# Optimization experiments

Measured on AMD Instinct MI355X. Metric: run time of the kernel, lower is better.

## Reference

```python
import jax, jax.numpy as jnp
import numpy as np

E = 1024
H = 16
DFF = 4 * E
EPS = 1e-5


def layer_norm(x, scale, bias):
    mu = jnp.mean(x, axis=-1, keepdims=True)
    var = jnp.var(x, axis=-1, keepdims=True)
    return (x - mu) * jax.lax.rsqrt(var + EPS) * scale + bias


def setup_inputs() -> dict:
    key = jax.random.key(0)
    ks = jax.random.split(key, 12)
    N, L = 2, 2048
    x = jax.random.normal(ks[0], (N, L, E), dtype=jnp.float32)
    attn_mask = jax.random.randint(ks[1], (N, H, L, L), 0, 2) == 1
    s = 0.02
    return {
        "x": x,
        "attn_mask": attn_mask,
        "ln1_s": jnp.ones((E,), jnp.float32),
        "ln1_b": jnp.zeros((E,), jnp.float32),
        "Wqkv": jax.random.normal(ks[2], (E, 3 * E), jnp.float32) * s,
        "bqkv": jnp.zeros((3 * E,), jnp.float32),
        "Wo": jax.random.normal(ks[3], (E, E), jnp.float32) * s,
        "bo": jnp.zeros((E,), jnp.float32),
        "ln2_s": jnp.ones((E,), jnp.float32),
        "ln2_b": jnp.zeros((E,), jnp.float32),
        "lnf_s": jnp.ones((E,), jnp.float32),
        "lnf_b": jnp.zeros((E,), jnp.float32),
        "W1": jax.random.normal(ks[4], (E, DFF), jnp.float32) * s,
        "b1": jnp.zeros((DFF,), jnp.float32),
        "W2": jax.random.normal(ks[5], (DFF, E), jnp.float32) * s,
        "b2": jnp.zeros((E,), jnp.float32),
    }


def reference(x, attn_mask, ln1_s, ln1_b, Wqkv, bqkv, Wo, bo,
              ln2_s, ln2_b, lnf_s, lnf_b, W1, b1, W2, b2):
    N, L, _ = x.shape
    D = E // H
    # --- self attention (pre-norm) ---
    h = layer_norm(x, ln1_s, ln1_b)
    qkv = h @ Wqkv + bqkv                      # [N,L,3E]
    q, k, v = jnp.split(qkv, 3, axis=-1)
    q = q.reshape(N, L, H, D)
    k = k.reshape(N, L, H, D)
    v = v.reshape(N, L, H, D)
    a = jnp.einsum('nqhd,nkhd->nhqk', q, k) * (D ** -0.5)  # [N,H,L,L]
    a = jnp.where(attn_mask, -jnp.inf, a)
    a = jax.nn.softmax(a, axis=-1)
    o = jnp.einsum('nhqk,nkhd->nqhd', a, v).reshape(N, L, E)
    o = o @ Wo + bo
    x = x + o
    # --- feedforward (norm_2 then FF's internal LN) ---
    h = layer_norm(x, ln2_s, ln2_b)
    h = layer_norm(h, lnf_s, lnf_b)
    h = jax.nn.gelu(h @ W1 + b1, approximate=False) @ W2 + b2
    return x + h
```

## Files before the change

### kernel.cpp

```cpp
#include <hip/hip_runtime.h>
#include <math.h>

#define E_DIM 1024
#define H_HEADS 16
#define D_HEAD 64
#define DFF_DIM 4096
#define L_SEQ 2048
#define N_BATCH 2
#define T_TOK (N_BATCH * L_SEQ)

typedef __attribute__((ext_vector_type(8))) __bf16 bf16x8;
typedef __attribute__((ext_vector_type(4))) float f32x4;

__device__ __forceinline__ unsigned short f2bf(float f) {
  union { float f; unsigned int u; } v; v.f = f;
  unsigned int r = v.u + 0x7fffu + ((v.u >> 16) & 1u);
  return (unsigned short)(r >> 16);
}

__device__ __forceinline__ void gld16(const void* g, void* l) {
  __builtin_amdgcn_global_load_lds(
      (const __attribute__((address_space(1))) unsigned int*)g,
      (__attribute__((address_space(3))) unsigned int*)l, 16, 0, 0);
}

__global__ __launch_bounds__(256) void convert_transpose(
    const float* __restrict__ in, unsigned short* __restrict__ out, int K, int N) {
  __shared__ float tile[32][33];
  int n0 = blockIdx.x * 32, k0 = blockIdx.y * 32;
  int tx = threadIdx.x & 31, ty = threadIdx.x >> 5;
#pragma unroll
  for (int i = 0; i < 32; i += 8)
    tile[ty + i][tx] = in[(size_t)(k0 + ty + i) * N + n0 + tx];
  __syncthreads();
#pragma unroll
  for (int i = 0; i < 32; i += 8)
    out[(size_t)(n0 + ty + i) * K + k0 + tx] = f2bf(tile[tx][ty + i]);
}

__global__ __launch_bounds__(256) void v_transpose(
    const unsigned short* __restrict__ qkv, unsigned short* __restrict__ vtg) {
  __shared__ unsigned short t[64][72];
  int kb = blockIdx.x * 64;
  int nh = blockIdx.y, n = nh >> 4, h = nh & 15;
  int tid = threadIdx.x;
  int r = tid >> 3, ch = tid & 7;
  const size_t TS = 3 * E_DIM;
  const size_t voff = 2 * E_DIM + h * 64;
#pragma unroll
  for (int it = 0; it < 2; it++) {
    int row = r + it * 32;
    uint4 v = *(const uint4*)(qkv + (size_t)(n * L_SEQ + kb + row) * TS + voff + ch * 8);
    *(uint4*)(&t[row][ch * 8]) = v;
  }
  __syncthreads();
#pragma unroll
  for (int it = 0; it < 2; it++) {
    int d = r + it * 32;
    unsigned short tmp[8];
#pragma unroll
    for (int s = 0; s < 8; s++) tmp[s] = t[ch * 8 + s][d];
    *(uint4*)(vtg + ((size_t)nh * 64 + d) * L_SEQ + kb + ch * 8) = *(uint4*)tmp;
  }
}

__device__ __forceinline__ void block_reduce2(float& a, float& b, float* sm, int tid) {
#pragma unroll
  for (int off = 32; off > 0; off >>= 1) {
    a += __shfl_down(a, off);
    b += __shfl_down(b, off);
  }
  int wid = tid >> 6;
  if ((tid & 63) == 0) { sm[wid * 2] = a; sm[wid * 2 + 1] = b; }
  __syncthreads();
  a = sm[0] + sm[2] + sm[4] + sm[6];
  b = sm[1] + sm[3] + sm[5] + sm[7];
}

__global__ __launch_bounds__(256) void ln_kernel(
    const float* __restrict__ x, const float* __restrict__ s,
    const float* __restrict__ b, unsigned short* __restrict__ out) {
  int row = blockIdx.x, tid = threadIdx.x;
  __shared__ float sm[8];
  float4 v = ((const float4*)(x + (size_t)row * E_DIM))[tid];
  float sum = v.x + v.y + v.z + v.w;
  float sq = v.x * v.x + v.y * v.y + v.z * v.z + v.w * v.w;
  block_reduce2(sum, sq, sm, tid);
  float mu = sum * (1.0f / E_DIM);
  float var = sq * (1.0f / E_DIM) - mu * mu;
  float rs = rsqrtf(var + 1e-5f);
  float4 sv = ((const float4*)s)[tid];
  float4 bv = ((const float4*)b)[tid];
  ushort4 o4;
  o4.x = f2bf((v.x - mu) * rs * sv.x + bv.x);
  o4.y = f2bf((v.y - mu) * rs * sv.y + bv.y);
  o4.z = f2bf((v.z - mu) * rs * sv.z + bv.z);
  o4.w = f2bf((v.w - mu) * rs * sv.w + bv.w);
  ((ushort4*)(out + (size_t)row * E_DIM))[tid] = o4;
}

__global__ __launch_bounds__(256) void ln2_fused_kernel(
    const float* __restrict__ p0, const float* __restrict__ p1,
    const float* __restrict__ x, const float* __restrict__ bo,
    const float* __restrict__ s2, const float* __restrict__ b2,
    const float* __restrict__ sf, const float* __restrict__ bf_,
    float* __restrict__ x2, unsigned short* __restrict__ out) {
  int row = blockIdx.x, tid = threadIdx.x;
  __shared__ float sm[8];
  float4 a0 = ((const float4*)(p0 + (size_t)row * E_DIM))[tid];
  float4 a1 = ((const float4*)(p1 + (size_t)row * E_DIM))[tid];
  float4 xv = ((const float4*)(x + (size_t)row * E_DIM))[tid];
  float4 bov = ((const float4*)bo)[tid];
  float4 v;
  v.x = a0.x + a1.x + xv.x + bov.x;
  v.y = a0.y + a1.y + xv.y + bov.y;
  v.z = a0.z + a1.z + xv.z + bov.z;
  v.w = a0.w + a1.w + xv.w + bov.w;
  ((float4*)(x2 + (size_t)row * E_DIM))[tid] = v;
  float sum = v.x + v.y + v.z + v.w;
  float sq = v.x * v.x + v.y * v.y + v.z * v.z + v.w * v.w;
  block_reduce2(sum, sq, sm, tid);
  float mu = sum * (1.0f / E_DIM);
  float rs = rsqrtf(sq * (1.0f / E_DIM) - mu * mu + 1e-5f);
  float4 s2v = ((const float4*)s2)[tid];
  float4 b2v = ((const float4*)b2)[tid];
  float y0 = (v.x - mu) * rs * s2v.x + b2v.x;
  float y1 = (v.y - mu) * rs * s2v.y + b2v.y;
  float y2 = (v.z - mu) * rs * s2v.z + b2v.z;
  float y3 = (v.w - mu) * rs * s2v.w + b2v.w;
  float sum2 = y0 + y1 + y2 + y3;
  float sq2 = y0 * y0 + y1 * y1 + y2 * y2 + y3 * y3;
  __syncthreads();
  block_reduce2(sum2, sq2, sm, tid);
  float mu2 = sum2 * (1.0f / E_DIM);
  float rs2 = rsqrtf(sq2 * (1.0f / E_DIM) - mu2 * mu2 + 1e-5f);
  float4 sfv = ((const float4*)sf)[tid];
  float4 bfv = ((const float4*)bf_)[tid];
  ushort4 o4;
  o4.x = f2bf((y0 - mu2) * rs2 * sfv.x + bfv.x);
  o4.y = f2bf((y1 - mu2) * rs2 * sfv.y + bfv.y);
  o4.z = f2bf((y2 - mu2) * rs2 * sfv.z + bfv.z);
  o4.w = f2bf((y3 - mu2) * rs2 * sfv.w + bfv.w);
  ((ushort4*)(out + (size_t)row * E_DIM))[tid] = o4;
}

__global__ __launch_bounds__(256) void add4_kernel(
    const float* __restrict__ p0, const float* __restrict__ p1,
    const float* __restrict__ p2, const float* __restrict__ p3,
    const float* __restrict__ resid, const float* __restrict__ bias,
    float* __restrict__ out) {
  int row = blockIdx.x, tid = threadIdx.x;
  size_t base = (size_t)row * E_DIM;
  float4 a0 = ((const float4*)(p0 + base))[tid];
  float4 a1 = ((const float4*)(p1 + base))[tid];
  float4 a2 = ((const float4*)(p2 + base))[tid];
  float4 a3 = ((const float4*)(p3 + base))[tid];
  float4 rv = ((const float4*)(resid + base))[tid];
  float4 bv = ((const float4*)bias)[tid];
  float4 o;
  o.x = a0.x + a1.x + a2.x + a3.x + rv.x + bv.x;
  o.y = a0.y + a1.y + a2.y + a3.y + rv.y + bv.y;
  o.z = a0.z + a1.z + a2.z + a3.z + rv.z + bv.z;
  o.w = a0.w + a1.w + a2.w + a3.w + rv.w + bv.w;
  ((float4*)(out + base))[tid] = o;
}

template <int EPI>
__global__ __launch_bounds__(256) void gemm_bt(
    const unsigned short* __restrict__ A, const unsigned short* __restrict__ Bt,
    const float* __restrict__ bias, void* __restrict__ outp,
    int M, int N, int K, int Ks) {
  __shared__ unsigned short As[128 * 32];
  __shared__ unsigned short Bs[128 * 32];
  int tid = threadIdx.x;
  int lane = tid & 63, wave = tid >> 6;
  int m0 = blockIdx.y * 128, n0 = blockIdx.x * 128;
  int kz = blockIdx.z * Ks;
  int wm = (wave & 1) * 64, wn = (wave >> 1) * 64;
  int lm = lane & 15, lq = lane >> 4;
  int srow = wave * 32 + (lane >> 2);
  int scol = (lane & 3) * 8;
  const unsigned short* Ag = A + (size_t)(m0 + srow) * K + scol;
  const unsigned short* Bg = Bt + (size_t)(n0 + srow) * K + scol;
  unsigned short* AsW = As + wave * 1024;
  unsigned short* BsW = Bs + wave * 1024;
  f32x4 acc[4][4] = {};
  for (int k0 = kz; k0 < kz + Ks; k0 += 32) {
    __syncthreads();
    gld16(Ag + k0, AsW);
    gld16(Ag + (size_t)16 * K + k0, AsW + 512);
    gld16(Bg + k0, BsW);
    gld16(Bg + (size_t)16 * K + k0, BsW + 512);
    __syncthreads();
    bf16x8 a[4], b[4];
#pragma unroll
    for (int i = 0; i < 4; i++)
      a[i] = *(const bf16x8*)(As + (wm + i * 16 + lm) * 32 + lq * 8);
#pragma unroll
    for (int j = 0; j < 4; j++)
      b[j] = *(const bf16x8*)(Bs + (wn + j * 16 + lm) * 32 + lq * 8);
#pragma unroll
    for (int i = 0; i < 4; i++)
#pragma unroll
      for (int j = 0; j < 4; j++)
        acc[i][j] = __builtin_amdgcn_mfma_f32_16x16x32_bf16(a[i], b[j], acc[i][j], 0, 0, 0);
  }
  float* pout = (EPI == 3) ? ((float*)outp + (size_t)blockIdx.z * M * N) : nullptr;
#pragma unroll
  for (int i = 0; i < 4; i++)
#pragma unroll
    for (int j = 0; j < 4; j++) {
      int row = m0 + wm + i * 16 + lq * 4;
      int col = n0 + wn + j * 16 + lm;
      float bcol = (EPI == 3) ? 0.0f : bias[col];
#pragma unroll
      for (int r = 0; r < 4; r++) {
        float v = acc[i][j][r] + bcol;
        size_t idx = (size_t)(row + r) * N + col;
        if (EPI == 0) {
          ((unsigned short*)outp)[idx] = f2bf(v);
        } else if (EPI == 1) {
          float g = 0.5f * v * (1.0f + erff(v * 0.70710678118f));
          ((unsigned short*)outp)[idx] = f2bf(g);
        } else {
          pout[idx] = v;
        }
      }
    }
}

__global__ __launch_bounds__(256) void attn_kernel(
    const unsigned short* __restrict__ qkv,
    const unsigned short* __restrict__ vtg,
    const int* __restrict__ mask,
    unsigned short* __restrict__ o) {
  const int bq = blockIdx.x;
  const int nh = blockIdx.y;
  const int h = nh & 15;
  const int tid = threadIdx.x, lane = tid & 63, wave = tid >> 6;
  const int lm = lane & 15, lq = lane >> 4, lm7 = lm & 7;

  __shared__ unsigned short Kb[2][64 * 64];
  __shared__ unsigned short Vb[2][64 * 64];
  __shared__ unsigned short Ps[4][16 * 64];

  const int q_base = bq * 64;
  const int tok0 = (nh >> 4) * L_SEQ;
  const int qoff = h * 64, koff = E_DIM + h * 64;
  const int* mbase = mask + (size_t)nh * L_SEQ * L_SEQ;
  const size_t TS = 3 * E_DIM;

  bf16x8 qf[2];
  {
    int t = tok0 + q_base + wave * 16 + lm;
    const unsigned short* qr = qkv + (size_t)t * TS + qoff + lq * 8;
    qf[0] = *(const bf16x8*)(qr);
    qf[1] = *(const bf16x8*)(qr + 32);
  }

  const int qrow = q_base + wave * 16 + lq * 4;
  const int lrow = lane >> 3;
  const int xch = ((lane & 7) ^ lrow) * 8;
  const unsigned short* kgb = qkv + koff + xch;
  const unsigned short* vgb = vtg + (size_t)nh * 64 * L_SEQ + xch;

  auto STAGE = [&](int buf, int kt) {
    int kb = kt * 64;
#pragma unroll
    for (int cc = 0; cc < 2; cc++) {
      int c = wave * 2 + cc;
      int row = c * 8 + lrow;
      gld16(kgb + (size_t)(tok0 + kb + row) * TS, Kb[buf] + c * 512);
      gld16(vgb + (size_t)row * L_SEQ + kb, Vb[buf] + c * 512);
    }
  };

  int mreg[16];
  auto load_m = [&](int kt) {
#pragma unroll
    for (int nt = 0; nt < 4; nt++)
#pragma unroll
      for (int r = 0; r < 4; r++)
        mreg[nt * 4 + r] =
            mbase[(size_t)(qrow + r) * L_SEQ + kt * 64 + nt * 16 + lm];
  };

  float m_run[4], l_run[4];
  f32x4 oacc[4] = {};
#pragma unroll
  for (int r = 0; r < 4; r++) { m_run[r] = -1e30f; l_run[r] = 0.0f; }

  STAGE(0, 0);
  load_m(0);
  __syncthreads();

  int cur = 0;
  const int NT = L_SEQ / 64;
  for (int kt = 0; kt < NT; kt++) {
    if (kt + 1 < NT) STAGE(cur ^ 1, kt + 1);

    f32x4 s[4];
    __builtin_amdgcn_s_setprio(1);
#pragma unroll
    for (int nt = 0; nt < 4; nt++) {
      int kidx = (nt * 16 + lm) * 64 + ((lq ^ lm7) << 3);
      bf16x8 kb0 = *(const bf16x8*)(Kb[cur] + kidx);
      bf16x8 kb1 = *(const bf16x8*)(Kb[cur] + (kidx ^ 32));
      f32x4 acc = {};
      acc = __builtin_amdgcn_mfma_f32_16x16x32_bf16(qf[0], kb0, acc, 0, 0, 0);
      acc = __builtin_amdgcn_mfma_f32_16x16x32_bf16(qf[1], kb1, acc, 0, 0, 0);
      s[nt] = acc;
    }
    __builtin_amdgcn_s_setprio(0);

#pragma unroll
    for (int nt = 0; nt < 4; nt++)
#pragma unroll
      for (int r = 0; r < 4; r++) {
        float v = s[nt][r] * 0.125f;
        s[nt][r] = mreg[nt * 4 + r] ? -1e30f : v;
      }
    load_m((kt + 1 < NT) ? kt + 1 : kt);

    float alpha[4], rsum[4];
#pragma unroll
    for (int r = 0; r < 4; r++) {
      float v = fmaxf(fmaxf(s[0][r], s[1][r]), fmaxf(s[2][r], s[3][r]));
#pragma unroll
      for (int mo = 1; mo < 16; mo <<= 1) v = fmaxf(v, __shfl_xor(v, mo));
      float mn = fmaxf(m_run[r], v);
      alpha[r] = __expf(m_run[r] - mn);
      m_run[r] = mn;
      rsum[r] = 0.0f;
    }
    unsigned short* pw = Ps[wave];
#pragma unroll
    for (int r = 0; r < 4; r++) {
      int prow = lq * 4 + r;
      int pbase = prow * 64 + lm7;
      int p7 = prow & 7;
#pragma unroll
      for (int nt = 0; nt < 4; nt++) {
        float p = __expf(s[nt][r] - m_run[r]);
        rsum[r] += p;
        pw[pbase + ((((nt << 1) | (lm >> 3)) ^ p7) << 3)] = f2bf(p);
      }
    }
#pragma unroll
    for (int r = 0; r < 4; r++) {
      float v = rsum[r];
#pragma unroll
      for (int mo = 1; mo < 16; mo <<= 1) v += __shfl_xor(v, mo);
      l_run[r] = l_run[r] * alpha[r] + v;
    }
#pragma unroll
    for (int j = 0; j < 4; j++)
#pragma unroll
      for (int r = 0; r < 4; r++) oacc[j][r] *= alpha[r];

    asm volatile("s_waitcnt lgkmcnt(0)" ::: "memory");
    __builtin_amdgcn_sched_barrier(0);

    __builtin_amdgcn_s_setprio(1);
#pragma unroll
    for (int c = 0; c < 2; c++) {
      int pc = ((((c << 2) | lq)) ^ lm7) << 3;
      bf16x8 pa = *(const bf16x8*)(pw + lm * 64 + pc);
#pragma unroll
      for (int j = 0; j < 4; j++) {
        bf16x8 vb = *(const bf16x8*)(Vb[cur] + (j * 16 + lm) * 64 + pc);
        oacc[j] = __builtin_amdgcn_mfma_f32_16x16x32_bf16(pa, vb, oacc[j], 0, 0, 0);
      }
    }
    __builtin_amdgcn_s_setprio(0);

    __syncthreads();
    cur ^= 1;
  }

#pragma unroll
  for (int r = 0; r < 4; r++) {
    float inv_l = 1.0f / l_run[r];
    int t = tok0 + qrow + r;
#pragma unroll
    for (int j = 0; j < 4; j++)
      o[(size_t)t * E_DIM + h * 64 + j * 16 + lm] = f2bf(oacc[j][r] * inv_l);
  }
}

extern "C" void kernel_launch(void* const* d_in, const int* in_sizes, int n_in,
                              void* d_out, int out_size, void* d_ws, size_t ws_size,
                              hipStream_t stream) {
  const float* x = (const float*)d_in[0];
  const int* mask = (const int*)d_in[1];
  const float* ln1_s = (const float*)d_in[2];
  const float* ln1_b = (const float*)d_in[3];
  const float* Wqkv = (const float*)d_in[4];
  const float* bqkv = (const float*)d_in[5];
  const float* Wo = (const float*)d_in[6];
  const float* bo = (const float*)d_in[7];
  const float* ln2_s = (const float*)d_in[8];
  const float* ln2_b = (const float*)d_in[9];
  const float* lnf_s = (const float*)d_in[10];
  const float* lnf_b = (const float*)d_in[11];
  const float* W1 = (const float*)d_in[12];
  const float* b1 = (const float*)d_in[13];
  const float* W2 = (const float*)d_in[14];
  const float* b2 = (const float*)d_in[15];

  size_t off = 0;
  auto alloc = [&](size_t bytes) {
    void* p = (char*)d_ws + off;
    off += (bytes + 255) & ~(size_t)255;
    return p;
  };
  unsigned short* WqkvT = (unsigned short*)alloc((size_t)3072 * 1024 * 2);
  unsigned short* WoT = (unsigned short*)alloc((size_t)1024 * 1024 * 2);
  unsigned short* W1T = (unsigned short*)alloc((size_t)4096 * 1024 * 2);
  unsigned short* W2T = (unsigned short*)alloc((size_t)1024 * 4096 * 2);
  unsigned short* h1 = (unsigned short*)alloc((size_t)T_TOK * E_DIM * 2);
  unsigned short* qkvb = (unsigned short*)alloc((size_t)T_TOK * 3 * E_DIM * 2);
  unsigned short* ob = (unsigned short*)alloc((size_t)T_TOK * E_DIM * 2);
  float* x2 = (float*)alloc((size_t)T_TOK * E_DIM * 4);
  unsigned short* h2 = (unsigned short*)alloc((size_t)T_TOK * E_DIM * 2);
  unsigned short* g1 = (unsigned short*)alloc((size_t)T_TOK * DFF_DIM * 2);
  float* part = (float*)alloc((size_t)4 * T_TOK * E_DIM * 4);
  unsigned short* vtg = (unsigned short*)alloc((size_t)T_TOK * E_DIM * 2);
  const size_t PSTRIDE = (size_t)T_TOK * E_DIM;

  convert_transpose<<<dim3(3072 / 32, 1024 / 32), 256, 0, stream>>>(Wqkv, WqkvT, 1024, 3072);
  convert_transpose<<<dim3(1024 / 32, 1024 / 32), 256, 0, stream>>>(Wo, WoT, 1024, 1024);
  convert_transpose<<<dim3(4096 / 32, 1024 / 32), 256, 0, stream>>>(W1, W1T, 1024, 4096);
  convert_transpose<<<dim3(1024 / 32, 4096 / 32), 256, 0, stream>>>(W2, W2T, 4096, 1024);
  ln_kernel<<<T_TOK, 256, 0, stream>>>(x, ln1_s, ln1_b, h1);
  gemm_bt<0><<<dim3(3072 / 128, T_TOK / 128, 1), 256, 0, stream>>>(
      h1, WqkvT, bqkv, qkvb, T_TOK, 3072, 1024, 1024);
  v_transpose<<<dim3(L_SEQ / 64, N_BATCH * H_HEADS), 256, 0, stream>>>(qkvb, vtg);
  attn_kernel<<<dim3(L_SEQ / 64, N_BATCH * H_HEADS), 256, 0, stream>>>(
      qkvb, vtg, mask, ob);
  gemm_bt<3><<<dim3(1024 / 128, T_TOK / 128, 2), 256, 0, stream>>>(
      ob, WoT, nullptr, part, T_TOK, 1024, 1024, 512);
  ln2_fused_kernel<<<T_TOK, 256, 0, stream>>>(
      part, part + PSTRIDE, x, bo, ln2_s, ln2_b, lnf_s, lnf_b, x2, h2);
  gemm_bt<1><<<dim3(DFF_DIM / 128, T_TOK / 128, 1), 256, 0, stream>>>(
      h2, W1T, b1, g1, T_TOK, DFF_DIM, 1024, 1024);
  gemm_bt<3><<<dim3(1024 / 128, T_TOK / 128, 4), 256, 0, stream>>>(
      g1, W2T, nullptr, part, T_TOK, 1024, 4096, 1024);
  add4_kernel<<<T_TOK, 256, 0, stream>>>(
      part, part + PSTRIDE, part + 2 * PSTRIDE, part + 3 * PSTRIDE,
      x2, b2, (float*)d_out);

  (void)in_sizes; (void)n_in; (void)out_size; (void)ws_size;
}
```

Measured before the change: 1.072 ms.

## Compute transposed S tiles and pass P via register shuffles instead of LDS

Swaps the MFMA operands so each lane holds four consecutive key columns of a single query row. This lets the mask load as int4 vectors, shrinks the row max and sum reductions to two cross-lane shuffles, and keeps a single running max and sum per lane. The probability tile is packed to bf16 and moved into the PV operand layout with ds_bpermute shuffles, removing the per-wave LDS P buffer and its wait. The cost is many more shuffle instructions, plus extra shuffles to broadcast alpha and l back to the output row layout.

```diff
diff --git a/kernel.cpp b/kernel.cpp
--- a/kernel.cpp
+++ b/kernel.cpp
@@ -242,7 +242,6 @@
 
   __shared__ unsigned short Kb[2][64 * 64];
   __shared__ unsigned short Vb[2][64 * 64];
-  __shared__ unsigned short Ps[4][16 * 64];
 
   const int q_base = bq * 64;
   const int tok0 = (nh >> 4) * L_SEQ;
@@ -258,7 +257,9 @@
     qf[1] = *(const bf16x8*)(qr + 32);
   }
 
-  const int qrow = q_base + wave * 16 + lq * 4;
+  const int qml = q_base + wave * 16 + lm;
+  const int qro = q_base + wave * 16 + lq * 4;
+
   const int lrow = lane >> 3;
   const int xch = ((lane & 7) ^ lrow) * 8;
   const unsigned short* kgb = qkv + koff + xch;
@@ -275,20 +276,21 @@
     }
   };
 
-  int mreg[16];
+  int4 mrg[4];
   auto load_m = [&](int kt) {
+    const int* mp = mbase + (size_t)qml * L_SEQ + kt * 64 + lq * 4;
 #pragma unroll
     for (int nt = 0; nt < 4; nt++)
-#pragma unroll
-      for (int r = 0; r < 4; r++)
-        mreg[nt * 4 + r] =
-            mbase[(size_t)(qrow + r) * L_SEQ + kt * 64 + nt * 16 + lm];
+      mrg[nt] = *(const int4*)(mp + nt * 16);
   };
 
-  float m_run[4], l_run[4];
+  const int s0 = (2 * lq) & 3;
+  const int srcA = lm + (s0 << 4);
+  const int srcB = lm + ((s0 + 1) << 4);
+  const int ntsel = lq >> 1;
+
+  float m_run = -1e30f, l_run = 0.0f;
   f32x4 oacc[4] = {};
-#pragma unroll
-  for (int r = 0; r < 4; r++) { m_run[r] = -1e30f; l_run[r] = 0.0f; }
 
   STAGE(0, 0);
   load_m(0);
@@ -307,65 +309,78 @@
       bf16x8 kb0 = *(const bf16x8*)(Kb[cur] + kidx);
       bf16x8 kb1 = *(const bf16x8*)(Kb[cur] + (kidx ^ 32));
       f32x4 acc = {};
-      acc = __builtin_amdgcn_mfma_f32_16x16x32_bf16(qf[0], kb0, acc, 0, 0, 0);
-      acc = __builtin_amdgcn_mfma_f32_16x16x32_bf16(qf[1], kb1, acc, 0, 0, 0);
+      acc = __builtin_amdgcn_mfma_f32_16x16x32_bf16(kb0, qf[0], acc, 0, 0, 0);
+      acc = __builtin_amdgcn_mfma_f32_16x16x32_bf16(kb1, qf[1], acc, 0, 0, 0);
       s[nt] = acc;
     }
     __builtin_amdgcn_s_setprio(0);
 
 #pragma unroll
-    for (int nt = 0; nt < 4; nt++)
-#pragma unroll
-      for (int r = 0; r < 4; r++) {
-        float v = s[nt][r] * 0.125f;
-        s[nt][r] = mreg[nt * 4 + r] ? -1e30f : v;
-      }
+    for (int nt = 0; nt < 4; nt++) {
+      s[nt][0] = mrg[nt].x ? -1e30f : s[nt][0] * 0.125f;
+      s[nt][1] = mrg[nt].y ? -1e30f : s[nt][1] * 0.125f;
+      s[nt][2] = mrg[nt].z ? -1e30f : s[nt][2] * 0.125f;
+      s[nt][3] = mrg[nt].w ? -1e30f : s[nt][3] * 0.125f;
+    }
     load_m((kt + 1 < NT) ? kt + 1 : kt);
 
-    float alpha[4], rsum[4];
-#pragma unroll
-    for (int r = 0; r < 4; r++) {
-      float v = fmaxf(fmaxf(s[0][r], s[1][r]), fmaxf(s[2][r], s[3][r]));
-#pragma unroll
-      for (int mo = 1; mo < 16; mo <<= 1) v = fmaxf(v, __shfl_xor(v, mo));
-      float mn = fmaxf(m_run[r], v);
-      alpha[r] = __expf(m_run[r] - mn);
-      m_run[r] = mn;
-      rsum[r] = 0.0f;
-    }
-    unsigned short* pw = Ps[wave];
-#pragma unroll
-    for (int r = 0; r < 4; r++) {
-      int prow = lq * 4 + r;
-      int pbase = prow * 64 + lm7;
-      int p7 = prow & 7;
-#pragma unroll
-      for (int nt = 0; nt < 4; nt++) {
-        float p = __expf(s[nt][r] - m_run[r]);
-        rsum[r] += p;
-        pw[pbase + ((((nt << 1) | (lm >> 3)) ^ p7) << 3)] = f2bf(p);
-      }
-    }
-#pragma unroll
-    for (int r = 0; r < 4; r++) {
-      float v = rsum[r];
-#pragma unroll
-      for (int mo = 1; mo < 16; mo <<= 1) v += __shfl_xor(v, mo);
-      l_run[r] = l_run[r] * alpha[r] + v;
-    }
+    float mx = fmaxf(fmaxf(s[0][0], s[0][1]), fmaxf(s[0][2], s[0][3]));
+#pragma unroll
+    for (int nt = 1; nt < 4; nt++)
+      mx = fmaxf(mx, fmaxf(fmaxf(s[nt][0], s[nt][1]), fmaxf(s[nt][2], s[nt][3])));
+    mx = fmaxf(mx, __shfl_xor(mx, 16));
+    mx = fmaxf(mx, __shfl_xor(mx, 32));
+    float mn = fmaxf(m_run, mx);
+    float alpha = __expf(m_run - mn);
+    m_run = mn;
+
+    unsigned int pk[4][2];
+    float rs = 0.0f;
+#pragma unroll
+    for (int nt = 0; nt < 4; nt++) {
+      float p0 = __expf(s[nt][0] - mn), p1 = __expf(s[nt][1] - mn);
+      float p2 = __expf(s[nt][2] - mn), p3 = __expf(s[nt][3] - mn);
+      rs += (p0 + p1) + (p2 + p3);
+      pk[nt][0] = (unsigned int)f2bf(p0) | ((unsigned int)f2bf(p1) << 16);
+      pk[nt][1] = (unsigned int)f2bf(p2) | ((unsigned int)f2bf(p3) << 16);
+    }
+    rs += __shfl_xor(rs, 16);
+    rs += __shfl_xor(rs, 32);
+    l_run = l_run * alpha + rs;
+
+    union PF { unsigned int w[4]; bf16x8 v; } pf0, pf1;
+    {
+      unsigned int a00 = __shfl((int)pk[0][0], srcA), a01 = __shfl((int)pk[0][1], srcA);
+      unsigned int a10 = __shfl((int)pk[1][0], srcA), a11 = __shfl((int)pk[1][1], srcA);
+      unsigned int b00 = __shfl((int)pk[0][0], srcB), b01 = __shfl((int)pk[0][1], srcB);
+      unsigned int b10 = __shfl((int)pk[1][0], srcB), b11 = __shfl((int)pk[1][1], srcB);
+      pf0.w[0] = ntsel ? a10 : a00;
+      pf0.w[1] = ntsel ? a11 : a01;
+      pf0.w[2] = ntsel ? b10 : b00;
+      pf0.w[3] = ntsel ? b11 : b01;
+      unsigned int c00 = __shfl((int)pk[2][0], srcA), c01 = __shfl((int)pk[2][1], srcA);
+      unsigned int c10 = __shfl((int)pk[3][0], srcA), c11 = __shfl((int)pk[3][1], srcA);
+      unsigned int d00 = __shfl((int)pk[2][0], srcB), d01 = __shfl((int)pk[2][1], srcB);
+      unsigned int d10 = __shfl((int)pk[3][0], srcB), d11 = __shfl((int)pk[3][1], srcB);
+      pf1.w[0] = ntsel ? c10 : c00;
+      pf1.w[1] = ntsel ? c11 : c01;
+      pf1.w[2] = ntsel ? d10 : d00;
+      pf1.w[3] = ntsel ? d11 : d01;
+    }
+
+    float af[4];
+#pragma unroll
+    for (int r = 0; r < 4; r++) af[r] = __shfl(alpha, qro - q_base - wave * 16 + r);
 #pragma unroll
     for (int j = 0; j < 4; j++)
 #pragma unroll
-      for (int r = 0; r < 4; r++) oacc[j][r] *= alpha[r];
-
-    asm volatile("s_waitcnt lgkmcnt(0)" ::: "memory");
-    __builtin_amdgcn_sched_barrier(0);
+      for (int r = 0; r < 4; r++) oacc[j][r] *= af[r];
 
     __builtin_amdgcn_s_setprio(1);
 #pragma unroll
     for (int c = 0; c < 2; c++) {
-      int pc = ((((c << 2) | lq)) ^ lm7) << 3;
-      bf16x8 pa = *(const bf16x8*)(pw + lm * 64 + pc);
+      bf16x8 pa = c ? pf1.v : pf0.v;
+      int pc = (((c << 2) | lq) ^ lm7) << 3;
 #pragma unroll
       for (int j = 0; j < 4; j++) {
         bf16x8 vb = *(const bf16x8*)(Vb[cur] + (j * 16 + lm) * 64 + pc);
@@ -380,8 +395,9 @@
 
 #pragma unroll
   for (int r = 0; r < 4; r++) {
-    float inv_l = 1.0f / l_run[r];
-    int t = tok0 + qrow + r;
+    float lr = __shfl(l_run, (lq * 4 + r));
+    float inv_l = 1.0f / lr;
+    int t = tok0 + qro + r;
 #pragma unroll
     for (int j = 0; j < 4; j++)
       o[(size_t)t * E_DIM + h * 64 + j * 16 + lm] = f2bf(oacc[j][r] * inv_l);
```

Result: faster. 1.036 ms (-3.4%).
